# Kernel tuning notes

Measured on AMD Instinct MI355X. Metric: run time of the kernel, lower is better.

The kernel has to match this reference:

```python
import jax, jax.numpy as jnp
import numpy as np

NUM_NODES = 10000
NODE_DIM = 128
EDGE_DIM = 128
HIDDEN_DIM = 128
OUT_DIM = 128
N_EDGES = 640000


def setup_inputs() -> dict:
    key = jax.random.key(0)
    k = jax.random.split(key, 8)
    x = jax.random.normal(k[0], (NUM_NODES, NODE_DIM), dtype=jnp.float32)
    edge_index = jax.random.randint(k[1], (2, N_EDGES), 0, NUM_NODES, dtype=jnp.int64)
    edge_attr = jax.random.normal(k[2], (N_EDGES, EDGE_DIM), dtype=jnp.float32)
    # node2edge linear: in = 2*node_dim + edge_dim
    s1 = 1.0 / np.sqrt(2 * NODE_DIM + EDGE_DIM)
    W1 = jax.random.uniform(k[3], (2 * NODE_DIM + EDGE_DIM, HIDDEN_DIM), jnp.float32, -s1, s1)
    b1 = jax.random.uniform(k[4], (HIDDEN_DIM,), jnp.float32, -s1, s1)
    # edge2node linear: in = hidden_dim + node_dim
    s2 = 1.0 / np.sqrt(HIDDEN_DIM + NODE_DIM)
    W2 = jax.random.uniform(k[5], (HIDDEN_DIM + NODE_DIM, OUT_DIM), jnp.float32, -s2, s2)
    b2 = jax.random.uniform(k[6], (OUT_DIM,), jnp.float32, -s2, s2)
    return {"x": x, "edge_index": edge_index, "edge_attr": edge_attr,
            "W1": W1, "b1": b1, "W2": W2, "b2": b2}


def reference(x, edge_index, edge_attr, W1, b1, W2, b2):
    src, dst = edge_index[0], edge_index[1]
    # Node2Edge: gather endpoints, concat with edge features, linear
    h_i = x[src]                                   # [E, node_dim]
    h_j = x[dst]                                   # [E, node_dim]
    inp_e = jnp.concatenate([h_i, h_j, edge_attr], axis=-1)  # [E, 2*nd+ed]
    h_edge = inp_e @ W1 + b1                       # [E, hidden]
    # Edge2Node: scatter-sum edge embeddings to target nodes (edge_index[1])
    agg = jax.ops.segment_sum(h_edge, dst, num_segments=NUM_NODES)  # [N, hidden]
    inp_n = jnp.concatenate([agg, x], axis=-1)     # [N, hidden+nd]
    h_node = inp_n @ W2 + b2                       # [N, out]
    return h_node
```

## Files before the change

### kernel.cpp

```cpp
#include <hip/hip_runtime.h>


#define NN 10000
#define ED 640000
#define D  128
#define NB 64
#define EPB (ED / NB)
#define ST 192

typedef __bf16 bf16;
typedef bf16  bf16x8 __attribute__((ext_vector_type(8)));
typedef float f32x4  __attribute__((ext_vector_type(4)));

__device__ __forceinline__ bf16 f2b(float f) {
  unsigned u = __builtin_bit_cast(unsigned, f);
  u += 0x7fffu + ((u >> 16) & 1u);
  unsigned short h = (unsigned short)(u >> 16);
  return __builtin_bit_cast(bf16, h);
}

__device__ __forceinline__ bf16x8 bzero8() {
  bf16 z = __builtin_bit_cast(bf16, (unsigned short)0);
  bf16x8 v = {z, z, z, z, z, z, z, z};
  return v;
}

__global__ __launch_bounds__(256) void k_prep_hist(const float* __restrict__ x,
                                                   const float* __restrict__ W1,
                                                   const float* __restrict__ W2,
                                                   const int*   __restrict__ dst,
                                                   bf16* __restrict__ xb,
                                                   bf16* __restrict__ W1p,
                                                   bf16* __restrict__ W2p,
                                                   int*  __restrict__ hist) {
  __shared__ __align__(16) int h[NN];
  int tid = threadIdx.x;
  if (blockIdx.x < NB) {
    int b = blockIdx.x;
    int4 z4 = make_int4(0, 0, 0, 0);
    for (int i = tid; i < NN / 4; i += 256) ((int4*)h)[i] = z4;
    __syncthreads();
    const int4* d4 = (const int4*)(dst + b * EPB);
    for (int i = tid; i < EPB / 4; i += 256) {
      int4 dd = d4[i];
      atomicAdd(&h[dd.x], 1);
      atomicAdd(&h[dd.y], 1);
      atomicAdd(&h[dd.z], 1);
      atomicAdd(&h[dd.w], 1);
    }
    __syncthreads();
    int4* outp = (int4*)(hist + (size_t)b * NN);
    for (int i = tid; i < NN / 4; i += 256) outp[i] = ((const int4*)h)[i];
    return;
  }
  int id = (blockIdx.x - NB) * 256 + tid;
  if (id < 160000) {
    int i = id * 8;
    f32x4 a = *(const f32x4*)(x + i);
    f32x4 b = *(const f32x4*)(x + i + 4);
    bf16x8 hh;
    hh[0]=f2b(a[0]); hh[1]=f2b(a[1]); hh[2]=f2b(a[2]); hh[3]=f2b(a[3]);
    hh[4]=f2b(b[0]); hh[5]=f2b(b[1]); hh[6]=f2b(b[2]); hh[7]=f2b(b[3]);
    *(bf16x8*)(xb + i) = hh;
  } else if (id < 166144) {
    int o8 = id - 160000;
    int kb = o8 >> 9, rem = o8 & 511, t = rem >> 6, L = rem & 63;
    int col  = t * 16 + (L & 15);
    int row0 = kb * 32 + (L >> 4) * 8;
    bf16x8 hh;
    #pragma unroll
    for (int j = 0; j < 8; j++) hh[j] = f2b(W1[(row0 + j) * D + col]);
    *(bf16x8*)(W1p + o8 * 8) = hh;
  } else if (id < 170240) {
    int o8 = id - 166144;
    int kb = o8 >> 9, rem = o8 & 511, t = rem >> 6, L = rem & 63;
    int col  = t * 16 + (L & 15);
    int row0 = kb * 32 + (L >> 4) * 8;
    bf16x8 hh;
    #pragma unroll
    for (int j = 0; j < 8; j++) hh[j] = f2b(W2[(row0 + j) * D + col]);
    *(bf16x8*)(W2p + o8 * 8) = hh;
  }
}

__global__ __launch_bounds__(256) void k_colscan(int* __restrict__ hist,
                                                 int* __restrict__ counts) {
  int v = blockIdx.x * 256 + threadIdx.x;
  if (v >= NN) return;
  int run = 0;
  #pragma unroll
  for (int b = 0; b < NB; b++) {
    int t = hist[b * NN + v];
    hist[b * NN + v] = run;
    run += t;
  }
  counts[v] = run;
}

__global__ __launch_bounds__(256) void k_fill(const int* __restrict__ src,
                                              const int* __restrict__ dst,
                                              const int* __restrict__ hist,
                                              int2* __restrict__ csr) {
  __shared__ __align__(16) int rk[NN];
  int b = blockIdx.x, tid = threadIdx.x;
  int4 z4 = make_int4(0, 0, 0, 0);
  for (int i = tid; i < NN / 4; i += 256) ((int4*)rk)[i] = z4;
  __syncthreads();
  int base = b * EPB;
  const int* __restrict__ hb = hist + (size_t)b * NN;
  const int4* d4 = (const int4*)(dst + base);
  const int4* s4 = (const int4*)(src + base);
  for (int i = tid; i < EPB / 4; i += 256) {
    int4 dd = d4[i];
    int4 ss = s4[i];
    int e = base + i * 4;
    {
      int r = atomicAdd(&rk[dd.x], 1);
      csr[(size_t)dd.x * ST + hb[dd.x] + r] = make_int2(e + 0, ss.x);
    }
    {
      int r = atomicAdd(&rk[dd.y], 1);
      csr[(size_t)dd.y * ST + hb[dd.y] + r] = make_int2(e + 1, ss.y);
    }
    {
      int r = atomicAdd(&rk[dd.z], 1);
      csr[(size_t)dd.z * ST + hb[dd.z] + r] = make_int2(e + 2, ss.z);
    }
    {
      int r = atomicAdd(&rk[dd.w], 1);
      csr[(size_t)dd.w * ST + hb[dd.w] + r] = make_int2(e + 3, ss.w);
    }
  }
}

__global__ __launch_bounds__(256) void k_sum(const bf16*  __restrict__ xb,
                                             const float* __restrict__ ea,
                                             const int*   __restrict__ counts,
                                             const int2*  __restrict__ csr,
                                             float* __restrict__ sx,
                                             float* __restrict__ sea) {
  int gwave = (blockIdx.x * 256 + threadIdx.x) >> 6;
  if (gwave >= NN) return;
  int lane = threadIdx.x & 63;
  int g = lane >> 4, l = lane & 15;
  int cnt = counts[gwave];
  const int2* cbase = csr + (size_t)gwave * ST;

  f32x4 ax0 = {0.f,0.f,0.f,0.f}, ax1 = {0.f,0.f,0.f,0.f};
  f32x4 ae0 = {0.f,0.f,0.f,0.f}, ae1 = {0.f,0.f,0.f,0.f};

  #pragma unroll 2
  for (int e = g; e < cnt; e += 4) {
    long long cp = __builtin_nontemporal_load((const long long*)(cbase + e));
    int2 es = __builtin_bit_cast(int2, cp);
    const f32x4* ep = (const f32x4*)(ea + (size_t)es.x * D + l * 8);
    f32x4 f0 = __builtin_nontemporal_load(ep);
    f32x4 f1 = __builtin_nontemporal_load(ep + 1);
    bf16x8 hx = *(const bf16x8*)(xb + (size_t)es.y * D + l * 8);
    ax0[0] += (float)hx[0]; ax0[1] += (float)hx[1];
    ax0[2] += (float)hx[2]; ax0[3] += (float)hx[3];
    ax1[0] += (float)hx[4]; ax1[1] += (float)hx[5];
    ax1[2] += (float)hx[6]; ax1[3] += (float)hx[7];
    ae0 += f0;
    ae1 += f1;
  }
  #pragma unroll
  for (int i = 0; i < 4; i++) {
    ax0[i] += __shfl_xor(ax0[i], 16, 64); ax0[i] += __shfl_xor(ax0[i], 32, 64);
    ax1[i] += __shfl_xor(ax1[i], 16, 64); ax1[i] += __shfl_xor(ax1[i], 32, 64);
    ae0[i] += __shfl_xor(ae0[i], 16, 64); ae0[i] += __shfl_xor(ae0[i], 32, 64);
    ae1[i] += __shfl_xor(ae1[i], 16, 64); ae1[i] += __shfl_xor(ae1[i], 32, 64);
  }
  if (lane < 16) {
    f32x4* px = (f32x4*)(sx  + (size_t)gwave * D + l * 8);
    f32x4* pe = (f32x4*)(sea + (size_t)gwave * D + l * 8);
    __builtin_nontemporal_store(ax0, px);
    __builtin_nontemporal_store(ax1, px + 1);
    __builtin_nontemporal_store(ae0, pe);
    __builtin_nontemporal_store(ae1, pe + 1);
  }
}

__global__ __launch_bounds__(256) void k_out(const float* __restrict__ sx,
                                             const float* __restrict__ sea,
                                             const bf16*  __restrict__ xb,
                                             const bf16*  __restrict__ W1p,
                                             const bf16*  __restrict__ W2p,
                                             const float* __restrict__ b1,
                                             const float* __restrict__ b2,
                                             const int*   __restrict__ counts,
                                             float* __restrict__ out) {
  __shared__ __align__(16) bf16 lds[64 * 392];
  int tid  = threadIdx.x;
  int wave = tid >> 6, lane = tid & 63, quad = lane >> 4, l16 = lane & 15;
  int n0 = blockIdx.x * 64;

  #pragma unroll
  for (int i = 0; i < 4; i++) {
    int m = (tid >> 4) + 16 * i;
    int v = n0 + m;
    int cl = tid & 15;
    float cntf = (v < NN) ? (float)counts[v] : 0.f;
    #pragma unroll
    for (int j = 0; j < 3; j++) {
      int c = cl + 16 * j;
      bf16x8 h;
      if (v < NN) {
        if (j == 0) {
          const f32x4* p = (const f32x4*)(sx + (size_t)v * D + cl * 8);
          f32x4 f0 = __builtin_nontemporal_load(p);
          f32x4 f1 = __builtin_nontemporal_load(p + 1);
          h[0]=f2b(f0[0]); h[1]=f2b(f0[1]); h[2]=f2b(f0[2]); h[3]=f2b(f0[3]);
          h[4]=f2b(f1[0]); h[5]=f2b(f1[1]); h[6]=f2b(f1[2]); h[7]=f2b(f1[3]);
        } else if (j == 1) {
          bf16x8 hx = *(const bf16x8*)(xb + (size_t)v * D + cl * 8);
          #pragma unroll
          for (int k = 0; k < 8; k++) h[k] = f2b((float)hx[k] * cntf);
        } else {
          const f32x4* p = (const f32x4*)(sea + (size_t)v * D + cl * 8);
          f32x4 f0 = __builtin_nontemporal_load(p);
          f32x4 f1 = __builtin_nontemporal_load(p + 1);
          h[0]=f2b(f0[0]); h[1]=f2b(f0[1]); h[2]=f2b(f0[2]); h[3]=f2b(f0[3]);
          h[4]=f2b(f1[0]); h[5]=f2b(f1[1]); h[6]=f2b(f1[2]); h[7]=f2b(f1[3]);
        }
      } else h = bzero8();
      *(bf16x8*)&lds[m * 392 + c * 8] = h;
    }
  }
  __syncthreads();

  f32x4 acc[4][2];
  #pragma unroll
  for (int mt = 0; mt < 4; mt++)
    #pragma unroll
    for (int tt = 0; tt < 2; tt++) acc[mt][tt] = (f32x4){0.f, 0.f, 0.f, 0.f};

  #pragma unroll
  for (int kb = 0; kb < 12; kb++) {
    bf16x8 B0 = *(const bf16x8*)(W1p + ((kb * 8 + wave * 2 + 0) * 64 + lane) * 8);
    bf16x8 B1 = *(const bf16x8*)(W1p + ((kb * 8 + wave * 2 + 1) * 64 + lane) * 8);
    #pragma unroll
    for (int mt = 0; mt < 4; mt++) {
      bf16x8 a = *(const bf16x8*)&lds[(mt * 16 + l16) * 392 + kb * 32 + quad * 8];
      acc[mt][0] = __builtin_amdgcn_mfma_f32_16x16x32_bf16(a, B0, acc[mt][0], 0, 0, 0);
      acc[mt][1] = __builtin_amdgcn_mfma_f32_16x16x32_bf16(a, B1, acc[mt][1], 0, 0, 0);
    }
  }
  __syncthreads();

  #pragma unroll
  for (int tt = 0; tt < 2; tt++) {
    int col = wave * 32 + tt * 16 + l16;
    float bb = b1[col];
    #pragma unroll
    for (int mt = 0; mt < 4; mt++)
      #pragma unroll
      for (int r = 0; r < 4; r++) {
        int m = mt * 16 + quad * 4 + r;
        int v = n0 + m;
        float cntf = (v < NN) ? (float)counts[v] : 0.f;
        lds[m * 264 + col] = f2b(acc[mt][tt][r] + cntf * bb);
      }
  }
  #pragma unroll
  for (int i = 0; i < 4; i++) {
    int m = (tid >> 4) + 16 * i;
    int c = tid & 15;
    int v = n0 + m;
    bf16x8 h = (v < NN) ? *(const bf16x8*)(xb + (size_t)v * D + c * 8) : bzero8();
    *(bf16x8*)&lds[m * 264 + 128 + c * 8] = h;
  }
  __syncthreads();

  f32x4 acc2[4][2];
  #pragma unroll
  for (int mt = 0; mt < 4; mt++)
    #pragma unroll
    for (int tt = 0; tt < 2; tt++) acc2[mt][tt] = (f32x4){0.f, 0.f, 0.f, 0.f};

  #pragma unroll
  for (int kb = 0; kb < 8; kb++) {
    bf16x8 B0 = *(const bf16x8*)(W2p + ((kb * 8 + wave * 2 + 0) * 64 + lane) * 8);
    bf16x8 B1 = *(const bf16x8*)(W2p + ((kb * 8 + wave * 2 + 1) * 64 + lane) * 8);
    #pragma unroll
    for (int mt = 0; mt < 4; mt++) {
      bf16x8 a = *(const bf16x8*)&lds[(mt * 16 + l16) * 264 + kb * 32 + quad * 8];
      acc2[mt][0] = __builtin_amdgcn_mfma_f32_16x16x32_bf16(a, B0, acc2[mt][0], 0, 0, 0);
      acc2[mt][1] = __builtin_amdgcn_mfma_f32_16x16x32_bf16(a, B1, acc2[mt][1], 0, 0, 0);
    }
  }

  #pragma unroll
  for (int tt = 0; tt < 2; tt++) {
    int col = wave * 32 + tt * 16 + l16;
    float bb = b2[col];
    #pragma unroll
    for (int mt = 0; mt < 4; mt++)
      #pragma unroll
      for (int r = 0; r < 4; r++) {
        int v = n0 + mt * 16 + quad * 4 + r;
        if (v < NN) out[(size_t)v * D + col] = acc2[mt][tt][r] + bb;
      }
  }
}

extern "C" void kernel_launch(void* const* d_in, const int* in_sizes, int n_in,
                              void* d_out, int out_size, void* d_ws, size_t ws_size,
                              hipStream_t stream) {
  const float* x  = (const float*)d_in[0];
  const int*   ei = (const int*)  d_in[1];
  const float* ea = (const float*)d_in[2];
  const float* W1 = (const float*)d_in[3];
  const float* b1 = (const float*)d_in[4];
  const float* W2 = (const float*)d_in[5];
  const float* b2 = (const float*)d_in[6];
  float* out = (float*)d_out;

  char* ws = (char*)d_ws;
  size_t off = 0;
  auto alloc = [&](size_t bytes) -> void* {
    void* p = ws + off;
    off += (bytes + 255) & ~(size_t)255;
    return p;
  };
  bf16*  xb      = (bf16*)alloc((size_t)NN * D * 2);
  bf16*  W1p     = (bf16*)alloc(49152 * 2);
  bf16*  W2p     = (bf16*)alloc(32768 * 2);
  float* sx      = (float*)alloc((size_t)NN * D * 4);
  float* sea     = (float*)alloc((size_t)NN * D * 4);
  int*   counts  = (int*)alloc(NN * 4);
  int*   hist    = (int*)alloc((size_t)NB * NN * 4);
  int2*  csr     = (int2*)alloc((size_t)NN * ST * 8);
  (void)ws_size; (void)in_sizes; (void)n_in; (void)out_size;

  const int* src = ei;
  const int* dst = ei + ED;

  k_prep_hist<<<NB + 665, 256, 0, stream>>>(x, W1, W2, dst, xb, W1p, W2p, hist);
  k_colscan<<<40, 256, 0, stream>>>(hist, counts);
  k_fill<<<NB, 256, 0, stream>>>(src, dst, hist, csr);
  k_sum<<<2500, 256, 0, stream>>>(xb, ea, counts, csr, sx, sea);
  k_out<<<157, 256, 0, stream>>>(sx, sea, xb, W1p, W2p, b1, b2, counts, out);
}
```

Baseline: 510.9 us.

## Fuse CSR build into one cooperative kernel and stage bf16 node inputs

Measured after the change: 563.6 us. +10.3%, slower.

```diff
diff --git a/kernel.cpp b/kernel.cpp
--- a/kernel.cpp
+++ b/kernel.cpp
@@ -1,4 +1,5 @@
 #include <hip/hip_runtime.h>
+#include <hip/hip_cooperative_groups.h>
 
 
 #define NN 10000
@@ -25,110 +26,103 @@
   return v;
 }
 
-__global__ __launch_bounds__(256) void k_prep_hist(const float* __restrict__ x,
-                                                   const float* __restrict__ W1,
-                                                   const float* __restrict__ W2,
-                                                   const int*   __restrict__ dst,
-                                                   bf16* __restrict__ xb,
-                                                   bf16* __restrict__ W1p,
-                                                   bf16* __restrict__ W2p,
-                                                   int*  __restrict__ hist) {
-  __shared__ __align__(16) int h[NN];
-  int tid = threadIdx.x;
-  if (blockIdx.x < NB) {
-    int b = blockIdx.x;
-    int4 z4 = make_int4(0, 0, 0, 0);
-    for (int i = tid; i < NN / 4; i += 256) ((int4*)h)[i] = z4;
-    __syncthreads();
-    const int4* d4 = (const int4*)(dst + b * EPB);
-    for (int i = tid; i < EPB / 4; i += 256) {
-      int4 dd = d4[i];
-      atomicAdd(&h[dd.x], 1);
-      atomicAdd(&h[dd.y], 1);
-      atomicAdd(&h[dd.z], 1);
-      atomicAdd(&h[dd.w], 1);
-    }
-    __syncthreads();
-    int4* outp = (int4*)(hist + (size_t)b * NN);
-    for (int i = tid; i < NN / 4; i += 256) outp[i] = ((const int4*)h)[i];
-    return;
-  }
-  int id = (blockIdx.x - NB) * 256 + tid;
+__global__ __launch_bounds__(256) void k_prep(const float* __restrict__ x,
+                                              const float* __restrict__ W1,
+                                              const float* __restrict__ W2,
+                                              bf16* __restrict__ xb,
+                                              bf16* __restrict__ W1p,
+                                              bf16* __restrict__ W2p) {
+  int id = blockIdx.x * 256 + threadIdx.x;
   if (id < 160000) {
     int i = id * 8;
     f32x4 a = *(const f32x4*)(x + i);
     f32x4 b = *(const f32x4*)(x + i + 4);
-    bf16x8 hh;
-    hh[0]=f2b(a[0]); hh[1]=f2b(a[1]); hh[2]=f2b(a[2]); hh[3]=f2b(a[3]);
-    hh[4]=f2b(b[0]); hh[5]=f2b(b[1]); hh[6]=f2b(b[2]); hh[7]=f2b(b[3]);
-    *(bf16x8*)(xb + i) = hh;
+    bf16x8 h;
+    h[0]=f2b(a[0]); h[1]=f2b(a[1]); h[2]=f2b(a[2]); h[3]=f2b(a[3]);
+    h[4]=f2b(b[0]); h[5]=f2b(b[1]); h[6]=f2b(b[2]); h[7]=f2b(b[3]);
+    *(bf16x8*)(xb + i) = h;
   } else if (id < 166144) {
     int o8 = id - 160000;
     int kb = o8 >> 9, rem = o8 & 511, t = rem >> 6, L = rem & 63;
     int col  = t * 16 + (L & 15);
     int row0 = kb * 32 + (L >> 4) * 8;
-    bf16x8 hh;
-    #pragma unroll
-    for (int j = 0; j < 8; j++) hh[j] = f2b(W1[(row0 + j) * D + col]);
-    *(bf16x8*)(W1p + o8 * 8) = hh;
+    bf16x8 h;
+    #pragma unroll
+    for (int j = 0; j < 8; j++) h[j] = f2b(W1[(row0 + j) * D + col]);
+    *(bf16x8*)(W1p + o8 * 8) = h;
   } else if (id < 170240) {
     int o8 = id - 166144;
     int kb = o8 >> 9, rem = o8 & 511, t = rem >> 6, L = rem & 63;
     int col  = t * 16 + (L & 15);
     int row0 = kb * 32 + (L >> 4) * 8;
-    bf16x8 hh;
-    #pragma unroll
-    for (int j = 0; j < 8; j++) hh[j] = f2b(W2[(row0 + j) * D + col]);
-    *(bf16x8*)(W2p + o8 * 8) = hh;
-  }
-}
-
-__global__ __launch_bounds__(256) void k_colscan(int* __restrict__ hist,
-                                                 int* __restrict__ counts) {
-  int v = blockIdx.x * 256 + threadIdx.x;
-  if (v >= NN) return;
-  int run = 0;
-  #pragma unroll
-  for (int b = 0; b < NB; b++) {
-    int t = hist[b * NN + v];
-    hist[b * NN + v] = run;
-    run += t;
-  }
-  counts[v] = run;
-}
-
-__global__ __launch_bounds__(256) void k_fill(const int* __restrict__ src,
-                                              const int* __restrict__ dst,
-                                              const int* __restrict__ hist,
-                                              int2* __restrict__ csr) {
-  __shared__ __align__(16) int rk[NN];
+    bf16x8 h;
+    #pragma unroll
+    for (int j = 0; j < 8; j++) h[j] = f2b(W2[(row0 + j) * D + col]);
+    *(bf16x8*)(W2p + o8 * 8) = h;
+  }
+}
+
+__global__ __launch_bounds__(256) void k_build(const int* __restrict__ src,
+                                               const int* __restrict__ dst,
+                                               int* __restrict__ hist,
+                                               int* __restrict__ counts,
+                                               int2* __restrict__ csr) {
+  cooperative_groups::grid_group grid = cooperative_groups::this_grid();
+  __shared__ __align__(16) int h[NN];
   int b = blockIdx.x, tid = threadIdx.x;
+
   int4 z4 = make_int4(0, 0, 0, 0);
-  for (int i = tid; i < NN / 4; i += 256) ((int4*)rk)[i] = z4;
-  __syncthreads();
-  int base = b * EPB;
-  const int* __restrict__ hb = hist + (size_t)b * NN;
-  const int4* d4 = (const int4*)(dst + base);
-  const int4* s4 = (const int4*)(src + base);
+  for (int i = tid; i < NN / 4; i += 256) ((int4*)h)[i] = z4;
+  __syncthreads();
+  const int4* d4 = (const int4*)(dst + b * EPB);
+  for (int i = tid; i < EPB / 4; i += 256) {
+    int4 dd = d4[i];
+    atomicAdd(&h[dd.x], 1);
+    atomicAdd(&h[dd.y], 1);
+    atomicAdd(&h[dd.z], 1);
+    atomicAdd(&h[dd.w], 1);
+  }
+  __syncthreads();
+  int4* outp = (int4*)(hist + (size_t)b * NN);
+  for (int i = tid; i < NN / 4; i += 256) outp[i] = ((const int4*)h)[i];
+  grid.sync();
+
+  int v = b * 256 + tid;
+  if (v < NN) {
+    int run = 0;
+    #pragma unroll
+    for (int bb = 0; bb < NB; bb++) {
+      int t = hist[bb * NN + v];
+      hist[bb * NN + v] = run;
+      run += t;
+    }
+    counts[v] = run;
+  }
+  grid.sync();
+
+  const int4* hp = (const int4*)(hist + (size_t)b * NN);
+  for (int i = tid; i < NN / 4; i += 256) ((int4*)h)[i] = hp[i];
+  __syncthreads();
+  const int4* s4 = (const int4*)(src + b * EPB);
   for (int i = tid; i < EPB / 4; i += 256) {
     int4 dd = d4[i];
     int4 ss = s4[i];
-    int e = base + i * 4;
+    int e = b * EPB + i * 4;
     {
-      int r = atomicAdd(&rk[dd.x], 1);
-      csr[(size_t)dd.x * ST + hb[dd.x] + r] = make_int2(e + 0, ss.x);
+      int r = atomicAdd(&h[dd.x], 1);
+      csr[(size_t)dd.x * ST + r] = make_int2(e + 0, ss.x);
     }
     {
-      int r = atomicAdd(&rk[dd.y], 1);
-      csr[(size_t)dd.y * ST + hb[dd.y] + r] = make_int2(e + 1, ss.y);
+      int r = atomicAdd(&h[dd.y], 1);
+      csr[(size_t)dd.y * ST + r] = make_int2(e + 1, ss.y);
     }
     {
-      int r = atomicAdd(&rk[dd.z], 1);
-      csr[(size_t)dd.z * ST + hb[dd.z] + r] = make_int2(e + 2, ss.z);
+      int r = atomicAdd(&h[dd.z], 1);
+      csr[(size_t)dd.z * ST + r] = make_int2(e + 2, ss.z);
     }
     {
-      int r = atomicAdd(&rk[dd.w], 1);
-      csr[(size_t)dd.w * ST + hb[dd.w] + r] = make_int2(e + 3, ss.w);
+      int r = atomicAdd(&h[dd.w], 1);
+      csr[(size_t)dd.w * ST + r] = make_int2(e + 3, ss.w);
     }
   }
 }
@@ -137,8 +131,7 @@
                                              const float* __restrict__ ea,
                                              const int*   __restrict__ counts,
                                              const int2*  __restrict__ csr,
-                                             float* __restrict__ sx,
-                                             float* __restrict__ sea) {
+                                             bf16* __restrict__ a1) {
   int gwave = (blockIdx.x * 256 + threadIdx.x) >> 6;
   if (gwave >= NN) return;
   int lane = threadIdx.x & 63;
@@ -171,18 +164,28 @@
     ae0[i] += __shfl_xor(ae0[i], 16, 64); ae0[i] += __shfl_xor(ae0[i], 32, 64);
     ae1[i] += __shfl_xor(ae1[i], 16, 64); ae1[i] += __shfl_xor(ae1[i], 32, 64);
   }
-  if (lane < 16) {
-    f32x4* px = (f32x4*)(sx  + (size_t)gwave * D + l * 8);
-    f32x4* pe = (f32x4*)(sea + (size_t)gwave * D + l * 8);
-    __builtin_nontemporal_store(ax0, px);
-    __builtin_nontemporal_store(ax1, px + 1);
-    __builtin_nontemporal_store(ae0, pe);
-    __builtin_nontemporal_store(ae1, pe + 1);
-  }
-}
-
-__global__ __launch_bounds__(256) void k_out(const float* __restrict__ sx,
-                                             const float* __restrict__ sea,
+  bf16* base = a1 + (size_t)gwave * 384;
+  if (g == 0) {
+    bf16x8 h;
+    h[0]=f2b(ax0[0]); h[1]=f2b(ax0[1]); h[2]=f2b(ax0[2]); h[3]=f2b(ax0[3]);
+    h[4]=f2b(ax1[0]); h[5]=f2b(ax1[1]); h[6]=f2b(ax1[2]); h[7]=f2b(ax1[3]);
+    __builtin_nontemporal_store(h, (bf16x8*)(base + l * 8));
+  } else if (g == 1) {
+    bf16x8 h;
+    h[0]=f2b(ae0[0]); h[1]=f2b(ae0[1]); h[2]=f2b(ae0[2]); h[3]=f2b(ae0[3]);
+    h[4]=f2b(ae1[0]); h[5]=f2b(ae1[1]); h[6]=f2b(ae1[2]); h[7]=f2b(ae1[3]);
+    __builtin_nontemporal_store(h, (bf16x8*)(base + 256 + l * 8));
+  } else if (g == 2) {
+    float cntf = (float)cnt;
+    bf16x8 hx = *(const bf16x8*)(xb + (size_t)gwave * D + l * 8);
+    bf16x8 h;
+    #pragma unroll
+    for (int k = 0; k < 8; k++) h[k] = f2b((float)hx[k] * cntf);
+    __builtin_nontemporal_store(h, (bf16x8*)(base + 128 + l * 8));
+  }
+}
+
+__global__ __launch_bounds__(256) void k_out(const bf16*  __restrict__ a1,
                                              const bf16*  __restrict__ xb,
                                              const bf16*  __restrict__ W1p,
                                              const bf16*  __restrict__ W2p,
@@ -200,30 +203,12 @@
     int m = (tid >> 4) + 16 * i;
     int v = n0 + m;
     int cl = tid & 15;
-    float cntf = (v < NN) ? (float)counts[v] : 0.f;
     #pragma unroll
     for (int j = 0; j < 3; j++) {
       int c = cl + 16 * j;
-      bf16x8 h;
-      if (v < NN) {
-        if (j == 0) {
-          const f32x4* p = (const f32x4*)(sx + (size_t)v * D + cl * 8);
-          f32x4 f0 = __builtin_nontemporal_load(p);
-          f32x4 f1 = __builtin_nontemporal_load(p + 1);
-          h[0]=f2b(f0[0]); h[1]=f2b(f0[1]); h[2]=f2b(f0[2]); h[3]=f2b(f0[3]);
-          h[4]=f2b(f1[0]); h[5]=f2b(f1[1]); h[6]=f2b(f1[2]); h[7]=f2b(f1[3]);
-        } else if (j == 1) {
-          bf16x8 hx = *(const bf16x8*)(xb + (size_t)v * D + cl * 8);
-          #pragma unroll
-          for (int k = 0; k < 8; k++) h[k] = f2b((float)hx[k] * cntf);
-        } else {
-          const f32x4* p = (const f32x4*)(sea + (size_t)v * D + cl * 8);
-          f32x4 f0 = __builtin_nontemporal_load(p);
-          f32x4 f1 = __builtin_nontemporal_load(p + 1);
-          h[0]=f2b(f0[0]); h[1]=f2b(f0[1]); h[2]=f2b(f0[2]); h[3]=f2b(f0[3]);
-          h[4]=f2b(f1[0]); h[5]=f2b(f1[1]); h[6]=f2b(f1[2]); h[7]=f2b(f1[3]);
-        }
-      } else h = bzero8();
+      bf16x8 h = bzero8();
+      if (v < NN)
+        h = __builtin_nontemporal_load((const bf16x8*)(a1 + (size_t)v * 384 + c * 8));
       *(bf16x8*)&lds[m * 392 + c * 8] = h;
     }
   }
@@ -326,8 +311,7 @@
   bf16*  xb      = (bf16*)alloc((size_t)NN * D * 2);
   bf16*  W1p     = (bf16*)alloc(49152 * 2);
   bf16*  W2p     = (bf16*)alloc(32768 * 2);
-  float* sx      = (float*)alloc((size_t)NN * D * 4);
-  float* sea     = (float*)alloc((size_t)NN * D * 4);
+  bf16*  a1      = (bf16*)alloc((size_t)NN * 384 * 2);
   int*   counts  = (int*)alloc(NN * 4);
   int*   hist    = (int*)alloc((size_t)NB * NN * 4);
   int2*  csr     = (int2*)alloc((size_t)NN * ST * 8);
@@ -336,9 +320,13 @@
   const int* src = ei;
   const int* dst = ei + ED;
 
-  k_prep_hist<<<NB + 665, 256, 0, stream>>>(x, W1, W2, dst, xb, W1p, W2p, hist);
-  k_colscan<<<40, 256, 0, stream>>>(hist, counts);
-  k_fill<<<NB, 256, 0, stream>>>(src, dst, hist, csr);
-  k_sum<<<2500, 256, 0, stream>>>(xb, ea, counts, csr, sx, sea);
-  k_out<<<157, 256, 0, stream>>>(sx, sea, xb, W1p, W2p, b1, b2, counts, out);
-}
+  k_prep<<<665, 256, 0, stream>>>(x, W1, W2, xb, W1p, W2p);
+  {
+    void* args[] = {(void*)&src, (void*)&dst, (void*)&hist,
+                    (void*)&counts, (void*)&csr};
+    hipLaunchCooperativeKernel((const void*)k_build, dim3(NB), dim3(256),
+                               args, 0, stream);
+  }
+  k_sum<<<2500, 256, 0, stream>>>(xb, ea, counts, csr, a1);
+  k_out<<<157, 256, 0, stream>>>(a1, xb, W1p, W2p, b1, b2, counts, out);
+}
```
